# Kernel tuning notes

Hardware: AMD Instinct MI355X
Metric: run time of the kernel (lower is better)

Reference implementation:

```python
import jax, jax.numpy as jnp
import numpy as np

TOP_K = 2


def setup_inputs() -> dict:
    key = jax.random.key(0)
    ks = jax.random.split(key, 5)
    T, H, I, E = 4096, 2048, 4096, 8
    scale = 0.02
    return {
        "hidden_states": jax.random.normal(ks[0], (T, H), dtype=jnp.float32),
        "router_logits": jax.random.normal(ks[1], (T, E), dtype=jnp.float32),
        "w1": jax.random.normal(ks[2], (E, I, H), dtype=jnp.float32) * scale,
        "w3": jax.random.normal(ks[3], (E, I, H), dtype=jnp.float32) * scale,
        "w2": jax.random.normal(ks[4], (E, H, I), dtype=jnp.float32) * scale,
    }


def reference(hidden_states, router_logits, w1, w3, w2):
    # hidden_states: [T, H], router_logits: [T, E]
    E = w1.shape[0]
    # Top-k routing with softmax renormalization over the selected logits.
    topk_vals, topk_idx = jax.lax.top_k(router_logits, TOP_K)  # [T, K]
    routing_weights = jax.nn.softmax(topk_vals, axis=-1)       # [T, K]
    # combine[t, e] = sum of routing weights of slots that picked expert e
    combine = jnp.sum(
        jnp.where(topk_idx[:, :, None] == jnp.arange(E)[None, None, :],
                  routing_weights[:, :, None], 0.0),
        axis=1)  # [T, E]
    out = jnp.zeros_like(hidden_states)
    for e in range(E):  # fixed small structural loop over experts
        gate = hidden_states @ w1[e].T        # [T, I]
        up = hidden_states @ w3[e].T          # [T, I]
        y = (jax.nn.silu(gate) * up) @ w2[e].T  # [T, H]
        out = out + combine[:, e, None] * y
    return out
```

## Files before the change

### kernel.cpp

```cpp
#include <hip/hip_runtime.h>
#include <stdint.h>

#define T_TOK 4096
#define H_DIM 2048
#define I_DIM 4096
#define N_EXP 8

typedef __attribute__((ext_vector_type(8))) short bf16x8;
typedef __attribute__((ext_vector_type(4))) float f32x4;
typedef __attribute__((ext_vector_type(8))) unsigned short u16x8;

__device__ __forceinline__ unsigned short f2bf(float x) {
    union { float f; unsigned u; } v; v.f = x;
    unsigned r = v.u + 0x7FFF + ((v.u >> 16) & 1);
    return (unsigned short)(r >> 16);
}

__device__ __forceinline__ void async_cp16(const void* g, const unsigned short* lds_base) {
    __builtin_amdgcn_global_load_lds(
        (const __attribute__((address_space(1))) unsigned*)g,
        (__attribute__((address_space(3))) unsigned*)(unsigned)(uintptr_t)lds_base,
        16, 0, 0);
}

__global__ void routing_kernel(const float* __restrict__ logits,
                               int* __restrict__ counts, int* __restrict__ offsets,
                               int* __restrict__ btok, float* __restrict__ bw,
                               int* __restrict__ tok2slot) {
    __shared__ int s_cnt[N_EXP];
    __shared__ int s_off[N_EXP];
    __shared__ int s_cur[N_EXP];
    const int tid = threadIdx.x;
    if (tid < N_EXP) s_cnt[tid] = 0;
    __syncthreads();

    int e0a[16], e1a[16]; float w0a[16], w1a[16];
    #pragma unroll
    for (int it = 0; it < 16; ++it) {
        int t = tid + it * 256;
        float l[8];
        #pragma unroll
        for (int e = 0; e < 8; ++e) l[e] = logits[t * 8 + e];
        int b0 = 0; float v0 = l[0];
        #pragma unroll
        for (int e = 1; e < 8; ++e) if (l[e] > v0) { v0 = l[e]; b0 = e; }
        int b1 = (b0 == 0) ? 1 : 0; float v1 = l[b1];
        #pragma unroll
        for (int e = 0; e < 8; ++e) if (e != b0 && l[e] > v1) { v1 = l[e]; b1 = e; }
        float w0 = 1.0f / (1.0f + __expf(v1 - v0));
        e0a[it] = b0; e1a[it] = b1; w0a[it] = w0; w1a[it] = 1.0f - w0;
        atomicAdd(&s_cnt[b0], 1);
        atomicAdd(&s_cnt[b1], 1);
    }
    __syncthreads();
    if (tid == 0) {
        int acc = 0;
        for (int e = 0; e < N_EXP; ++e) { s_off[e] = acc; s_cur[e] = acc; acc += s_cnt[e]; }
    }
    __syncthreads();
    if (tid < N_EXP) { counts[tid] = s_cnt[tid]; offsets[tid] = s_off[tid]; }
    #pragma unroll
    for (int it = 0; it < 16; ++it) {
        int t = tid + it * 256;
        int p0 = atomicAdd(&s_cur[e0a[it]], 1);
        btok[p0] = t; bw[p0] = w0a[it];
        int p1 = atomicAdd(&s_cur[e1a[it]], 1);
        btok[p1] = t; bw[p1] = w1a[it];
        tok2slot[2 * t] = p0;
        tok2slot[2 * t + 1] = p1;
    }
}

__global__ void cvt_kernel(const float* __restrict__ x, unsigned short* __restrict__ xb) {
    int i = blockIdx.x * blockDim.x + threadIdx.x;
    float4 v = ((const float4*)x)[i];
    ushort4 o;
    o.x = f2bf(v.x); o.y = f2bf(v.y); o.z = f2bf(v.z); o.w = f2bf(v.w);
    ((ushort4*)xb)[i] = o;
}


__global__ __launch_bounds__(512, 2)
void gemm1p_kernel(const unsigned short* __restrict__ Xb,
                   const unsigned short* __restrict__ W1b,
                   const unsigned short* __restrict__ W3b,
                   const int* __restrict__ counts,
                   const int* __restrict__ offsets,
                   const int* __restrict__ btok,
                   unsigned short* __restrict__ hbuf) {
    const int e = blockIdx.z;
    const int ne = counts[e];
    const int mt = blockIdx.y;
    if (mt * 256 >= ne) return;
    const int nt = blockIdx.x;
    const int off = offsets[e];

    __shared__ unsigned short sA[3][256 * 32];
    __shared__ unsigned short sB1[3][128 * 32];
    __shared__ unsigned short sB3[3][128 * 32];
    __shared__ int s_tok[256];

    const int tid = threadIdx.x;
    if (tid < 256) {
        int slot = mt * 256 + tid;
        s_tok[tid] = btok[off + ((slot < ne) ? slot : (ne - 1))];
    }
    __syncthreads();

    const int lane = tid & 63;
    const int wv = tid >> 6;
    const int wm = (wv >> 1) << 6;
    const int wn = (wv & 1) << 6;
    const int q = lane >> 4;
    const int c = lane & 15;
    const int xq = q ^ ((c >> 1) & 3);

    const int aoff = (wm + c) * 32 + xq * 8;
    const int boff = (wn + c) * 32 + xq * 8;

    const int srow = wv * 16 + (lane >> 2);
    const int sg = (lane & 3) ^ ((lane >> 3) & 3);

    const unsigned short* gA0 = Xb + (size_t)s_tok[srow] * H_DIM + sg * 8;
    const unsigned short* gA1 = Xb + (size_t)s_tok[srow + 128] * H_DIM + sg * 8;
    const size_t wrow = (size_t)e * I_DIM + nt * 128 + srow;
    const unsigned short* gB1 = W1b + wrow * H_DIM + sg * 8;
    const unsigned short* gB3 = W3b + wrow * H_DIM + sg * 8;

    const int dofsA0 = wv * 512;
    const int dofsA1 = 4096 + wv * 512;
    const int dofsB  = wv * 512;

    f32x4 accg[4][4], accu[4][4];
    const f32x4 zero = {0.0f, 0.0f, 0.0f, 0.0f};
    #pragma unroll
    for (int i = 0; i < 4; ++i)
        #pragma unroll
        for (int j = 0; j < 4; ++j) { accg[i][j] = zero; accu[i][j] = zero; }

    async_cp16(gA0,      &sA[0][dofsA0]);
    async_cp16(gB1,      &sB1[0][dofsB]);
    async_cp16(gA1,      &sA[0][dofsA1]);
    async_cp16(gB3,      &sB3[0][dofsB]);
    async_cp16(gA0 + 32, &sA[1][dofsA0]);
    async_cp16(gB1 + 32, &sB1[1][dofsB]);
    async_cp16(gA1 + 32, &sA[1][dofsA1]);
    async_cp16(gB3 + 32, &sB3[1][dofsB]);
    asm volatile("s_waitcnt vmcnt(4)" ::: "memory");
    __builtin_amdgcn_s_barrier();
    __builtin_amdgcn_sched_barrier(0);

    const int NT = H_DIM / 32;
    for (int t = 0; t < NT; ++t) {
        const int cur = t % 3;
        const int nx2 = (t + 2) % 3;
        const bool stg = (t + 2) < NT;
        const int kt2 = (t + 2) * 32;

        bf16x8 af[4], b1f[4];
        #pragma unroll
        for (int i = 0; i < 4; ++i) af[i] = *(const bf16x8*)(&sA[cur][aoff + i * 512]);
        #pragma unroll
        for (int j = 0; j < 4; ++j) b1f[j] = *(const bf16x8*)(&sB1[cur][boff + j * 512]);
        if (stg) {
            async_cp16(gA0 + kt2, &sA[nx2][dofsA0]);
            async_cp16(gB1 + kt2, &sB1[nx2][dofsB]);
        }
        __builtin_amdgcn_s_barrier();
        __builtin_amdgcn_s_setprio(1);
        #pragma unroll
        for (int i = 0; i < 4; ++i)
            #pragma unroll
            for (int j = 0; j < 4; ++j)
                accg[i][j] = __builtin_amdgcn_mfma_f32_16x16x32_bf16(af[i], b1f[j], accg[i][j], 0, 0, 0);
        __builtin_amdgcn_s_setprio(0);
        __builtin_amdgcn_s_barrier();

        bf16x8 b3f[4];
        #pragma unroll
        for (int j = 0; j < 4; ++j) b3f[j] = *(const bf16x8*)(&sB3[cur][boff + j * 512]);
        if (stg) {
            async_cp16(gA1 + kt2, &sA[nx2][dofsA1]);
            async_cp16(gB3 + kt2, &sB3[nx2][dofsB]);
        }
        __builtin_amdgcn_s_barrier();
        __builtin_amdgcn_s_setprio(1);
        #pragma unroll
        for (int i = 0; i < 4; ++i)
            #pragma unroll
            for (int j = 0; j < 4; ++j)
                accu[i][j] = __builtin_amdgcn_mfma_f32_16x16x32_bf16(af[i], b3f[j], accu[i][j], 0, 0, 0);
        __builtin_amdgcn_s_setprio(0);

        if (t + 1 < NT) {
            if (stg) asm volatile("s_waitcnt vmcnt(4)" ::: "memory");
            else     asm volatile("s_waitcnt vmcnt(0)" ::: "memory");
            __builtin_amdgcn_s_barrier();
            __builtin_amdgcn_sched_barrier(0);
        }
    }

    #pragma unroll
    for (int i = 0; i < 4; ++i) {
        #pragma unroll
        for (int r = 0; r < 4; ++r) {
            int mloc = wm + i * 16 + q * 4 + r;
            int slot = mt * 256 + mloc;
            if (slot < ne) {
                size_t rowbase = (size_t)(off + slot) * I_DIM + nt * 128 + wn;
                #pragma unroll
                for (int j = 0; j < 4; ++j) {
                    float g = accg[i][j][r];
                    float u = accu[i][j][r];
                    float val = (g / (1.0f + __expf(-g))) * u;
                    hbuf[rowbase + j * 16 + c] = f2bf(val);
                }
            }
        }
    }
}

__global__ __launch_bounds__(512, 2)
void gemm2p_kernel(const unsigned short* __restrict__ hbuf,
                   const unsigned short* __restrict__ W2b,
                   const int* __restrict__ counts,
                   const int* __restrict__ offsets,
                   float* __restrict__ ybuf) {
    const int e = blockIdx.z;
    const int ne = counts[e];
    const int mt = blockIdx.y;
    if (mt * 256 >= ne) return;
    const int nt = blockIdx.x;
    const int off = offsets[e];

    __shared__ unsigned short sA[3][256 * 32];
    __shared__ unsigned short sB[3][256 * 32];

    const int tid = threadIdx.x;
    const int lane = tid & 63;
    const int wv = tid >> 6;
    const int wm = (wv >> 2) << 7;
    const int wn = (wv & 3) << 6;
    const int q = lane >> 4;
    const int c = lane & 15;
    const int xq = q ^ ((c >> 1) & 3);

    const int aoff = (wm + c) * 32 + xq * 8;
    const int boff = (wn + c) * 32 + xq * 8;

    const int srow = wv * 16 + (lane >> 2);
    const int sg = (lane & 3) ^ ((lane >> 3) & 3);

    int slot0 = mt * 256 + srow;        if (slot0 >= ne) slot0 = ne - 1;
    int slot1 = mt * 256 + srow + 128;  if (slot1 >= ne) slot1 = ne - 1;
    const unsigned short* gA0 = hbuf + (size_t)(off + slot0) * I_DIM + sg * 8;
    const unsigned short* gA1 = hbuf + (size_t)(off + slot1) * I_DIM + sg * 8;
    const size_t wrow = (size_t)e * H_DIM + nt * 256 + srow;
    const unsigned short* gB0 = W2b + wrow * I_DIM + sg * 8;
    const unsigned short* gB1 = W2b + (wrow + 128) * I_DIM + sg * 8;

    const int dofs0 = wv * 512;
    const int dofs1 = 4096 + wv * 512;

    f32x4 acc[8][4];
    const f32x4 zero = {0.0f, 0.0f, 0.0f, 0.0f};
    #pragma unroll
    for (int i = 0; i < 8; ++i)
        #pragma unroll
        for (int j = 0; j < 4; ++j) acc[i][j] = zero;

    async_cp16(gA0,      &sA[0][dofs0]);
    async_cp16(gB0,      &sB[0][dofs0]);
    async_cp16(gA1,      &sA[0][dofs1]);
    async_cp16(gB1,      &sB[0][dofs1]);
    async_cp16(gA0 + 32, &sA[1][dofs0]);
    async_cp16(gB0 + 32, &sB[1][dofs0]);
    async_cp16(gA1 + 32, &sA[1][dofs1]);
    async_cp16(gB1 + 32, &sB[1][dofs1]);
    asm volatile("s_waitcnt vmcnt(4)" ::: "memory");
    __builtin_amdgcn_s_barrier();
    __builtin_amdgcn_sched_barrier(0);

    const int NT = I_DIM / 32;
    for (int t = 0; t < NT; ++t) {
        const int cur = t % 3;
        const int nx2 = (t + 2) % 3;
        const bool stg = (t + 2) < NT;
        const int kt2 = (t + 2) * 32;

        bf16x8 af[4], bfr[4];
        #pragma unroll
        for (int i = 0; i < 4; ++i) af[i] = *(const bf16x8*)(&sA[cur][aoff + i * 512]);
        #pragma unroll
        for (int j = 0; j < 4; ++j) bfr[j] = *(const bf16x8*)(&sB[cur][boff + j * 512]);
        if (stg) {
            async_cp16(gA0 + kt2, &sA[nx2][dofs0]);
            async_cp16(gB0 + kt2, &sB[nx2][dofs0]);
        }
        __builtin_amdgcn_s_barrier();
        __builtin_amdgcn_s_setprio(1);
        #pragma unroll
        for (int i = 0; i < 4; ++i)
            #pragma unroll
            for (int j = 0; j < 4; ++j)
                acc[i][j] = __builtin_amdgcn_mfma_f32_16x16x32_bf16(af[i], bfr[j], acc[i][j], 0, 0, 0);
        __builtin_amdgcn_s_setprio(0);
        __builtin_amdgcn_s_barrier();

        bf16x8 af2[4];
        #pragma unroll
        for (int i = 0; i < 4; ++i) af2[i] = *(const bf16x8*)(&sA[cur][aoff + (i + 4) * 512]);
        if (stg) {
            async_cp16(gA1 + kt2, &sA[nx2][dofs1]);
            async_cp16(gB1 + kt2, &sB[nx2][dofs1]);
        }
        __builtin_amdgcn_s_barrier();
        __builtin_amdgcn_s_setprio(1);
        #pragma unroll
        for (int i = 0; i < 4; ++i)
            #pragma unroll
            for (int j = 0; j < 4; ++j)
                acc[i + 4][j] = __builtin_amdgcn_mfma_f32_16x16x32_bf16(af2[i], bfr[j], acc[i + 4][j], 0, 0, 0);
        __builtin_amdgcn_s_setprio(0);

        if (t + 1 < NT) {
            if (stg) asm volatile("s_waitcnt vmcnt(4)" ::: "memory");
            else     asm volatile("s_waitcnt vmcnt(0)" ::: "memory");
            __builtin_amdgcn_s_barrier();
            __builtin_amdgcn_sched_barrier(0);
        }
    }

    #pragma unroll
    for (int i = 0; i < 8; ++i) {
        #pragma unroll
        for (int r = 0; r < 4; ++r) {
            int mloc = wm + i * 16 + q * 4 + r;
            int slot = mt * 256 + mloc;
            if (slot < ne) {
                float* obase = ybuf + (size_t)(off + slot) * H_DIM + nt * 256 + wn;
                #pragma unroll
                for (int j = 0; j < 4; ++j)
                    obase[j * 16 + c] = acc[i][j][r];
            }
        }
    }
}

__global__ void combine_kernel(const float* __restrict__ ybuf,
                               const float* __restrict__ bw,
                               const int* __restrict__ tok2slot,
                               float* __restrict__ out) {
    int i = blockIdx.x * blockDim.x + threadIdx.x;
    int t = i >> 9;
    int h4 = i & 511;
    int p0 = tok2slot[2 * t], p1 = tok2slot[2 * t + 1];
    float w0 = bw[p0], w1 = bw[p1];
    float4 a = ((const float4*)(ybuf + (size_t)p0 * H_DIM))[h4];
    float4 b = ((const float4*)(ybuf + (size_t)p1 * H_DIM))[h4];
    float4 o;
    o.x = w0 * a.x + w1 * b.x;
    o.y = w0 * a.y + w1 * b.y;
    o.z = w0 * a.z + w1 * b.z;
    o.w = w0 * a.w + w1 * b.w;
    ((float4*)(out + (size_t)t * H_DIM))[h4] = o;
}


__global__ __launch_bounds__(256, 2)
void gemm1_kernel(const unsigned short* __restrict__ Xb,
                  const float* __restrict__ W1,
                  const float* __restrict__ W3,
                  const int* __restrict__ counts,
                  const int* __restrict__ offsets,
                  const int* __restrict__ btok,
                  unsigned short* __restrict__ hbuf) {
    const int e = blockIdx.z;
    const int ne = counts[e];
    const int mt = blockIdx.y;
    if (mt * 128 >= ne) return;
    const int nt = blockIdx.x;
    const int off = offsets[e];

    __shared__ unsigned short sA[128][32];
    __shared__ unsigned short sB1[128][32];
    __shared__ unsigned short sB3[128][32];
    __shared__ int s_tok[128];

    const int tid = threadIdx.x;
    if (tid < 128) {
        int slot = mt * 128 + tid;
        s_tok[tid] = (slot < ne) ? btok[off + slot] : -1;
    }

    const float* __restrict__ pB1 = W1 + (size_t)e * I_DIM * H_DIM + (size_t)(nt * 128) * H_DIM;
    const float* __restrict__ pB3 = W3 + (size_t)e * I_DIM * H_DIM + (size_t)(nt * 128) * H_DIM;

    const int lane = tid & 63;
    const int wv = tid >> 6;
    const int wm = (wv >> 1) << 6;
    const int wn = (wv & 1) << 6;
    const int q = lane >> 4;
    const int c = lane & 15;

    f32x4 accg[4][4], accu[4][4];
    const f32x4 zero = {0.0f, 0.0f, 0.0f, 0.0f};
    #pragma unroll
    for (int i = 0; i < 4; ++i)
        #pragma unroll
        for (int j = 0; j < 4; ++j) { accg[i][j] = zero; accu[i][j] = zero; }

    const int srow = tid >> 2;
    const int schunk = (tid & 3) * 8;

    for (int kt = 0; kt < H_DIM; kt += 32) {
        __syncthreads();
        #pragma unroll
        for (int p = 0; p < 2; ++p) {
            int r = srow + p * 64;
            int tok = s_tok[r];
            u16x8 av = {0, 0, 0, 0, 0, 0, 0, 0};
            if (tok >= 0)
                av = *(const u16x8*)(Xb + (size_t)tok * H_DIM + kt + schunk);
            *(u16x8*)(&sA[r][schunk]) = av;

            const float* b1 = pB1 + (size_t)r * H_DIM + kt + schunk;
            float4 x0 = *(const float4*)(b1);
            float4 x1 = *(const float4*)(b1 + 4);
            u16x8 bv;
            bv[0] = f2bf(x0.x); bv[1] = f2bf(x0.y); bv[2] = f2bf(x0.z); bv[3] = f2bf(x0.w);
            bv[4] = f2bf(x1.x); bv[5] = f2bf(x1.y); bv[6] = f2bf(x1.z); bv[7] = f2bf(x1.w);
            *(u16x8*)(&sB1[r][schunk]) = bv;

            const float* b3 = pB3 + (size_t)r * H_DIM + kt + schunk;
            float4 y0 = *(const float4*)(b3);
            float4 y1 = *(const float4*)(b3 + 4);
            u16x8 cv;
            cv[0] = f2bf(y0.x); cv[1] = f2bf(y0.y); cv[2] = f2bf(y0.z); cv[3] = f2bf(y0.w);
            cv[4] = f2bf(y1.x); cv[5] = f2bf(y1.y); cv[6] = f2bf(y1.z); cv[7] = f2bf(y1.w);
            *(u16x8*)(&sB3[r][schunk]) = cv;
        }
        __syncthreads();

        bf16x8 af[4], b1f[4], b3f[4];
        #pragma unroll
        for (int i = 0; i < 4; ++i)
            af[i] = *(const bf16x8*)(&sA[wm + i * 16 + c][q * 8]);
        #pragma unroll
        for (int j = 0; j < 4; ++j) {
            b1f[j] = *(const bf16x8*)(&sB1[wn + j * 16 + c][q * 8]);
            b3f[j] = *(const bf16x8*)(&sB3[wn + j * 16 + c][q * 8]);
        }
        #pragma unroll
        for (int i = 0; i < 4; ++i)
            #pragma unroll
            for (int j = 0; j < 4; ++j) {
                accg[i][j] = __builtin_amdgcn_mfma_f32_16x16x32_bf16(af[i], b1f[j], accg[i][j], 0, 0, 0);
                accu[i][j] = __builtin_amdgcn_mfma_f32_16x16x32_bf16(af[i], b3f[j], accu[i][j], 0, 0, 0);
            }
    }

    #pragma unroll
    for (int i = 0; i < 4; ++i) {
        #pragma unroll
        for (int r = 0; r < 4; ++r) {
            int mloc = wm + i * 16 + q * 4 + r;
            int slot = mt * 128 + mloc;
            if (slot < ne) {
                size_t rowbase = (size_t)(off + slot) * I_DIM + nt * 128 + wn;
                #pragma unroll
                for (int j = 0; j < 4; ++j) {
                    float g = accg[i][j][r];
                    float u = accu[i][j][r];
                    float val = (g / (1.0f + __expf(-g))) * u;
                    hbuf[rowbase + j * 16 + c] = f2bf(val);
                }
            }
        }
    }
}

__global__ __launch_bounds__(256, 2)
void gemm2_kernel(const unsigned short* __restrict__ hbuf,
                  const float* __restrict__ W2,
                  const int* __restrict__ counts,
                  const int* __restrict__ offsets,
                  const int* __restrict__ btok,
                  const float* __restrict__ bw,
                  float* __restrict__ out) {
    const int e = blockIdx.z;
    const int ne = counts[e];
    const int mt = blockIdx.y;
    if (mt * 128 >= ne) return;
    const int nt = blockIdx.x;
    const int off = offsets[e];

    __shared__ unsigned short sA[128][32];
    __shared__ unsigned short sB[128][32];

    const int tid = threadIdx.x;
    const int lane = tid & 63;
    const int wv = tid >> 6;
    const int wm = (wv >> 1) << 6;
    const int wn = (wv & 1) << 6;
    const int q = lane >> 4;
    const int c = lane & 15;

    const float* __restrict__ pB = W2 + (size_t)e * H_DIM * I_DIM + (size_t)(nt * 128) * I_DIM;

    f32x4 acc[4][4];
    const f32x4 zero = {0.0f, 0.0f, 0.0f, 0.0f};
    #pragma unroll
    for (int i = 0; i < 4; ++i)
        #pragma unroll
        for (int j = 0; j < 4; ++j) acc[i][j] = zero;

    const int srow = tid >> 2;
    const int schunk = (tid & 3) * 8;

    for (int kt = 0; kt < I_DIM; kt += 32) {
        __syncthreads();
        #pragma unroll
        for (int p = 0; p < 2; ++p) {
            int r = srow + p * 64;
            int slot = mt * 128 + r;
            u16x8 av = {0, 0, 0, 0, 0, 0, 0, 0};
            if (slot < ne)
                av = *(const u16x8*)(hbuf + (size_t)(off + slot) * I_DIM + kt + schunk);
            *(u16x8*)(&sA[r][schunk]) = av;

            const float* b = pB + (size_t)r * I_DIM + kt + schunk;
            float4 x0 = *(const float4*)(b);
            float4 x1 = *(const float4*)(b + 4);
            u16x8 bv;
            bv[0] = f2bf(x0.x); bv[1] = f2bf(x0.y); bv[2] = f2bf(x0.z); bv[3] = f2bf(x0.w);
            bv[4] = f2bf(x1.x); bv[5] = f2bf(x1.y); bv[6] = f2bf(x1.z); bv[7] = f2bf(x1.w);
            *(u16x8*)(&sB[r][schunk]) = bv;
        }
        __syncthreads();

        bf16x8 af[4], bfr[4];
        #pragma unroll
        for (int i = 0; i < 4; ++i)
            af[i] = *(const bf16x8*)(&sA[wm + i * 16 + c][q * 8]);
        #pragma unroll
        for (int j = 0; j < 4; ++j)
            bfr[j] = *(const bf16x8*)(&sB[wn + j * 16 + c][q * 8]);
        #pragma unroll
        for (int i = 0; i < 4; ++i)
            #pragma unroll
            for (int j = 0; j < 4; ++j)
                acc[i][j] = __builtin_amdgcn_mfma_f32_16x16x32_bf16(af[i], bfr[j], acc[i][j], 0, 0, 0);
    }

    #pragma unroll
    for (int i = 0; i < 4; ++i) {
        #pragma unroll
        for (int r = 0; r < 4; ++r) {
            int mloc = wm + i * 16 + q * 4 + r;
            int slot = mt * 128 + mloc;
            if (slot < ne) {
                int tok = btok[off + slot];
                float wgt = bw[off + slot];
                float* obase = out + (size_t)tok * H_DIM + nt * 128 + wn;
                #pragma unroll
                for (int j = 0; j < 4; ++j)
                    atomicAdd(obase + j * 16 + c, wgt * acc[i][j][r]);
            }
        }
    }
}


extern "C" void kernel_launch(void* const* d_in, const int* in_sizes, int n_in,
                              void* d_out, int out_size, void* d_ws, size_t ws_size,
                              hipStream_t stream) {
    const float* hs = (const float*)d_in[0];
    const float* rl = (const float*)d_in[1];
    const float* w1 = (const float*)d_in[2];
    const float* w3 = (const float*)d_in[3];
    const float* w2 = (const float*)d_in[4];
    float* out = (float*)d_out;

    char* ws = (char*)d_ws;
    int*   counts   = (int*)(ws);
    int*   offsets  = (int*)(ws + 256);
    int*   btok     = (int*)(ws + 4096);
    float* bw       = (float*)(ws + 36864);
    int*   tok2slot = (int*)(ws + 69632);

    const size_t MB = 1ull << 20;
    const size_t NEED_A = 529 * MB;

    if (ws_size >= NEED_A) {
        unsigned short* Xb   = (unsigned short*)(ws + 1 * MB);
        unsigned short* hbuf = (unsigned short*)(ws + 17 * MB);
        float*          ybuf = (float*)(ws + 81 * MB);
        unsigned short* w1b  = (unsigned short*)(ws + 145 * MB);
        unsigned short* w3b  = (unsigned short*)(ws + 273 * MB);
        unsigned short* w2b  = (unsigned short*)(ws + 401 * MB);

        routing_kernel<<<1, 256, 0, stream>>>(rl, counts, offsets, btok, bw, tok2slot);

        cvt_kernel<<<(T_TOK * H_DIM / 4) / 256, 256, 0, stream>>>(hs, Xb);
        int wn4 = N_EXP * I_DIM * H_DIM / 4;
        cvt_kernel<<<wn4 / 256, 256, 0, stream>>>(w1, w1b);
        cvt_kernel<<<wn4 / 256, 256, 0, stream>>>(w3, w3b);
        cvt_kernel<<<wn4 / 256, 256, 0, stream>>>(w2, w2b);

        gemm1p_kernel<<<dim3(I_DIM / 128, 32, N_EXP), 512, 0, stream>>>(
            Xb, w1b, w3b, counts, offsets, btok, hbuf);

        gemm2p_kernel<<<dim3(H_DIM / 256, 32, N_EXP), 512, 0, stream>>>(
            hbuf, w2b, counts, offsets, ybuf);

        combine_kernel<<<(T_TOK * (H_DIM / 4)) / 256, 256, 0, stream>>>(
            ybuf, bw, tok2slot, out);
    } else {
        unsigned short* Xb   = (unsigned short*)(ws + 1 * MB);
        unsigned short* hbuf = (unsigned short*)(ws + 32 * MB);

        hipMemsetAsync(out, 0, (size_t)T_TOK * H_DIM * sizeof(float), stream);

        routing_kernel<<<1, 256, 0, stream>>>(rl, counts, offsets, btok, bw, tok2slot);

        cvt_kernel<<<(T_TOK * H_DIM / 4) / 256, 256, 0, stream>>>(hs, Xb);

        gemm1_kernel<<<dim3(I_DIM / 128, T_TOK / 128, N_EXP), 256, 0, stream>>>(
            Xb, w1, w3, counts, offsets, btok, hbuf);

        gemm2_kernel<<<dim3(H_DIM / 128, T_TOK / 128, N_EXP), 256, 0, stream>>>(
            hbuf, w2, counts, offsets, btok, bw, out);
    }
}
```

Measured before the change: 1.276 ms.

## Deepen MoE GEMM pipelines to 4 stages and shrink gemm2 N-tile

Both grouped GEMM kernels move from a 3-buffer LDS ring with split half-iterations and extra barriers to a 4-buffer ring that prefetches three K-steps ahead, with one barrier per iteration. gemm1 reads token indices directly from global memory instead of staging them through shared memory with a syncthreads. gemm2's N tile drops from 256 to 128, so per-wave accumulators halve and the grid doubles. LDS use grows in gemm1, which may limit the two-blocks-per-CU occupancy, and the smaller gemm2 tile reloads the activation rows more often.

```diff
diff --git a/kernel.cpp b/kernel.cpp
--- a/kernel.cpp
+++ b/kernel.cpp
@@ -95,18 +95,11 @@
     const int nt = blockIdx.x;
     const int off = offsets[e];
 
-    __shared__ unsigned short sA[3][256 * 32];
-    __shared__ unsigned short sB1[3][128 * 32];
-    __shared__ unsigned short sB3[3][128 * 32];
-    __shared__ int s_tok[256];
+    __shared__ unsigned short sA[4][256 * 32];
+    __shared__ unsigned short sB1[4][128 * 32];
+    __shared__ unsigned short sB3[4][128 * 32];
 
     const int tid = threadIdx.x;
-    if (tid < 256) {
-        int slot = mt * 256 + tid;
-        s_tok[tid] = btok[off + ((slot < ne) ? slot : (ne - 1))];
-    }
-    __syncthreads();
-
     const int lane = tid & 63;
     const int wv = tid >> 6;
     const int wm = (wv >> 1) << 6;
@@ -121,8 +114,13 @@
     const int srow = wv * 16 + (lane >> 2);
     const int sg = (lane & 3) ^ ((lane >> 3) & 3);
 
-    const unsigned short* gA0 = Xb + (size_t)s_tok[srow] * H_DIM + sg * 8;
-    const unsigned short* gA1 = Xb + (size_t)s_tok[srow + 128] * H_DIM + sg * 8;
+    int sl0 = mt * 256 + srow;        if (sl0 >= ne) sl0 = ne - 1;
+    int sl1 = mt * 256 + srow + 128;  if (sl1 >= ne) sl1 = ne - 1;
+    const int tok0 = btok[off + sl0];
+    const int tok1 = btok[off + sl1];
+
+    const unsigned short* gA0 = Xb + (size_t)tok0 * H_DIM + sg * 8;
+    const unsigned short* gA1 = Xb + (size_t)tok1 * H_DIM + sg * 8;
     const size_t wrow = (size_t)e * I_DIM + nt * 128 + srow;
     const unsigned short* gB1 = W1b + wrow * H_DIM + sg * 8;
     const unsigned short* gB3 = W3b + wrow * H_DIM + sg * 8;
@@ -138,53 +136,48 @@
         #pragma unroll
         for (int j = 0; j < 4; ++j) { accg[i][j] = zero; accu[i][j] = zero; }
 
-    async_cp16(gA0,      &sA[0][dofsA0]);
-    async_cp16(gB1,      &sB1[0][dofsB]);
-    async_cp16(gA1,      &sA[0][dofsA1]);
-    async_cp16(gB3,      &sB3[0][dofsB]);
-    async_cp16(gA0 + 32, &sA[1][dofsA0]);
-    async_cp16(gB1 + 32, &sB1[1][dofsB]);
-    async_cp16(gA1 + 32, &sA[1][dofsA1]);
-    async_cp16(gB3 + 32, &sB3[1][dofsB]);
-    asm volatile("s_waitcnt vmcnt(4)" ::: "memory");
+    #pragma unroll
+    for (int h = 0; h < 3; ++h) {
+        const int k = h * 32;
+        async_cp16(gA0 + k, &sA[h][dofsA0]);
+        async_cp16(gA1 + k, &sA[h][dofsA1]);
+        async_cp16(gB1 + k, &sB1[h][dofsB]);
+        async_cp16(gB3 + k, &sB3[h][dofsB]);
+    }
+    asm volatile("s_waitcnt vmcnt(8)" ::: "memory");
     __builtin_amdgcn_s_barrier();
     __builtin_amdgcn_sched_barrier(0);
 
     const int NT = H_DIM / 32;
-    for (int t = 0; t < NT; ++t) {
-        const int cur = t % 3;
-        const int nx2 = (t + 2) % 3;
-        const bool stg = (t + 2) < NT;
-        const int kt2 = (t + 2) * 32;
-
-        bf16x8 af[4], b1f[4];
-        #pragma unroll
-        for (int i = 0; i < 4; ++i) af[i] = *(const bf16x8*)(&sA[cur][aoff + i * 512]);
-        #pragma unroll
-        for (int j = 0; j < 4; ++j) b1f[j] = *(const bf16x8*)(&sB1[cur][boff + j * 512]);
-        if (stg) {
-            async_cp16(gA0 + kt2, &sA[nx2][dofsA0]);
-            async_cp16(gB1 + kt2, &sB1[nx2][dofsB]);
-        }
-        __builtin_amdgcn_s_barrier();
+    #pragma unroll 4
+    for (int h = 0; h < NT; ++h) {
+        const unsigned short* pA  = sA[h & 3];
+        const unsigned short* pB1 = sB1[h & 3];
+        const unsigned short* pB3 = sB3[h & 3];
+
+        bf16x8 af[4], b1f[4], b3f[4];
+        #pragma unroll
+        for (int i = 0; i < 4; ++i) af[i]  = *(const bf16x8*)(pA  + aoff + i * 512);
+        #pragma unroll
+        for (int j = 0; j < 4; ++j) b1f[j] = *(const bf16x8*)(pB1 + boff + j * 512);
+        #pragma unroll
+        for (int j = 0; j < 4; ++j) b3f[j] = *(const bf16x8*)(pB3 + boff + j * 512);
+
+        if (h + 3 < NT) {
+            const int r3 = (h + 3) & 3;
+            const int k3 = (h + 3) * 32;
+            async_cp16(gA0 + k3, &sA[r3][dofsA0]);
+            async_cp16(gA1 + k3, &sA[r3][dofsA1]);
+            async_cp16(gB1 + k3, &sB1[r3][dofsB]);
+            async_cp16(gB3 + k3, &sB3[r3][dofsB]);
+        }
+
         __builtin_amdgcn_s_setprio(1);
         #pragma unroll
         for (int i = 0; i < 4; ++i)
             #pragma unroll
             for (int j = 0; j < 4; ++j)
                 accg[i][j] = __builtin_amdgcn_mfma_f32_16x16x32_bf16(af[i], b1f[j], accg[i][j], 0, 0, 0);
-        __builtin_amdgcn_s_setprio(0);
-        __builtin_amdgcn_s_barrier();
-
-        bf16x8 b3f[4];
-        #pragma unroll
-        for (int j = 0; j < 4; ++j) b3f[j] = *(const bf16x8*)(&sB3[cur][boff + j * 512]);
-        if (stg) {
-            async_cp16(gA1 + kt2, &sA[nx2][dofsA1]);
-            async_cp16(gB3 + kt2, &sB3[nx2][dofsB]);
-        }
-        __builtin_amdgcn_s_barrier();
-        __builtin_amdgcn_s_setprio(1);
         #pragma unroll
         for (int i = 0; i < 4; ++i)
             #pragma unroll
@@ -192,9 +185,10 @@
                 accu[i][j] = __builtin_amdgcn_mfma_f32_16x16x32_bf16(af[i], b3f[j], accu[i][j], 0, 0, 0);
         __builtin_amdgcn_s_setprio(0);
 
-        if (t + 1 < NT) {
-            if (stg) asm volatile("s_waitcnt vmcnt(4)" ::: "memory");
-            else     asm volatile("s_waitcnt vmcnt(0)" ::: "memory");
+        if (h + 1 < NT) {
+            if (h + 3 < NT)      asm volatile("s_waitcnt vmcnt(8)" ::: "memory");
+            else if (h + 2 < NT) asm volatile("s_waitcnt vmcnt(4)" ::: "memory");
+            else                 asm volatile("s_waitcnt vmcnt(0)" ::: "memory");
             __builtin_amdgcn_s_barrier();
             __builtin_amdgcn_sched_barrier(0);
         }
@@ -233,14 +227,14 @@
     const int nt = blockIdx.x;
     const int off = offsets[e];
 
-    __shared__ unsigned short sA[3][256 * 32];
-    __shared__ unsigned short sB[3][256 * 32];
+    __shared__ unsigned short sA[4][256 * 32];
+    __shared__ unsigned short sB[4][128 * 32];
 
     const int tid = threadIdx.x;
     const int lane = tid & 63;
     const int wv = tid >> 6;
-    const int wm = (wv >> 2) << 7;
-    const int wn = (wv & 3) << 6;
+    const int wm = (wv >> 1) << 6;
+    const int wn = (wv & 1) << 6;
     const int q = lane >> 4;
     const int c = lane & 15;
     const int xq = q ^ ((c >> 1) & 3);
@@ -255,49 +249,51 @@
     int slot1 = mt * 256 + srow + 128;  if (slot1 >= ne) slot1 = ne - 1;
     const unsigned short* gA0 = hbuf + (size_t)(off + slot0) * I_DIM + sg * 8;
     const unsigned short* gA1 = hbuf + (size_t)(off + slot1) * I_DIM + sg * 8;
-    const size_t wrow = (size_t)e * H_DIM + nt * 256 + srow;
-    const unsigned short* gB0 = W2b + wrow * I_DIM + sg * 8;
-    const unsigned short* gB1 = W2b + (wrow + 128) * I_DIM + sg * 8;
-
-    const int dofs0 = wv * 512;
-    const int dofs1 = 4096 + wv * 512;
-
-    f32x4 acc[8][4];
+    const size_t wrow = (size_t)e * H_DIM + nt * 128 + srow;
+    const unsigned short* gB = W2b + wrow * I_DIM + sg * 8;
+
+    const int dofsA0 = wv * 512;
+    const int dofsA1 = 4096 + wv * 512;
+    const int dofsB  = wv * 512;
+
+    f32x4 acc[4][4];
     const f32x4 zero = {0.0f, 0.0f, 0.0f, 0.0f};
     #pragma unroll
-    for (int i = 0; i < 8; ++i)
+    for (int i = 0; i < 4; ++i)
         #pragma unroll
         for (int j = 0; j < 4; ++j) acc[i][j] = zero;
 
-    async_cp16(gA0,      &sA[0][dofs0]);
-    async_cp16(gB0,      &sB[0][dofs0]);
-    async_cp16(gA1,      &sA[0][dofs1]);
-    async_cp16(gB1,      &sB[0][dofs1]);
-    async_cp16(gA0 + 32, &sA[1][dofs0]);
-    async_cp16(gB0 + 32, &sB[1][dofs0]);
-    async_cp16(gA1 + 32, &sA[1][dofs1]);
-    async_cp16(gB1 + 32, &sB[1][dofs1]);
-    asm volatile("s_waitcnt vmcnt(4)" ::: "memory");
+    #pragma unroll
+    for (int h = 0; h < 3; ++h) {
+        const int k = h * 32;
+        async_cp16(gA0 + k, &sA[h][dofsA0]);
+        async_cp16(gA1 + k, &sA[h][dofsA1]);
+        async_cp16(gB + k,  &sB[h][dofsB]);
+    }
+    asm volatile("s_waitcnt vmcnt(6)" ::: "memory");
     __builtin_amdgcn_s_barrier();
     __builtin_amdgcn_sched_barrier(0);
 
     const int NT = I_DIM / 32;
-    for (int t = 0; t < NT; ++t) {
-        const int cur = t % 3;
-        const int nx2 = (t + 2) % 3;
-        const bool stg = (t + 2) < NT;
-        const int kt2 = (t + 2) * 32;
+    #pragma unroll 4
+    for (int h = 0; h < NT; ++h) {
+        const unsigned short* pA = sA[h & 3];
+        const unsigned short* pB = sB[h & 3];
 
         bf16x8 af[4], bfr[4];
         #pragma unroll
-        for (int i = 0; i < 4; ++i) af[i] = *(const bf16x8*)(&sA[cur][aoff + i * 512]);
-        #pragma unroll
-        for (int j = 0; j < 4; ++j) bfr[j] = *(const bf16x8*)(&sB[cur][boff + j * 512]);
-        if (stg) {
-            async_cp16(gA0 + kt2, &sA[nx2][dofs0]);
-            async_cp16(gB0 + kt2, &sB[nx2][dofs0]);
-        }
-        __builtin_amdgcn_s_barrier();
+        for (int i = 0; i < 4; ++i) af[i]  = *(const bf16x8*)(pA + aoff + i * 512);
+        #pragma unroll
+        for (int j = 0; j < 4; ++j) bfr[j] = *(const bf16x8*)(pB + boff + j * 512);
+
+        if (h + 3 < NT) {
+            const int r3 = (h + 3) & 3;
+            const int k3 = (h + 3) * 32;
+            async_cp16(gA0 + k3, &sA[r3][dofsA0]);
+            async_cp16(gA1 + k3, &sA[r3][dofsA1]);
+            async_cp16(gB + k3,  &sB[r3][dofsB]);
+        }
+
         __builtin_amdgcn_s_setprio(1);
         #pragma unroll
         for (int i = 0; i < 4; ++i)
@@ -305,40 +301,24 @@
             for (int j = 0; j < 4; ++j)
                 acc[i][j] = __builtin_amdgcn_mfma_f32_16x16x32_bf16(af[i], bfr[j], acc[i][j], 0, 0, 0);
         __builtin_amdgcn_s_setprio(0);
-        __builtin_amdgcn_s_barrier();
-
-        bf16x8 af2[4];
-        #pragma unroll
-        for (int i = 0; i < 4; ++i) af2[i] = *(const bf16x8*)(&sA[cur][aoff + (i + 4) * 512]);
-        if (stg) {
-            async_cp16(gA1 + kt2, &sA[nx2][dofs1]);
-            async_cp16(gB1 + kt2, &sB[nx2][dofs1]);
-        }
-        __builtin_amdgcn_s_barrier();
-        __builtin_amdgcn_s_setprio(1);
-        #pragma unroll
-        for (int i = 0; i < 4; ++i)
-            #pragma unroll
-            for (int j = 0; j < 4; ++j)
-                acc[i + 4][j] = __builtin_amdgcn_mfma_f32_16x16x32_bf16(af2[i], bfr[j], acc[i + 4][j], 0, 0, 0);
-        __builtin_amdgcn_s_setprio(0);
-
-        if (t + 1 < NT) {
-            if (stg) asm volatile("s_waitcnt vmcnt(4)" ::: "memory");
-            else     asm volatile("s_waitcnt vmcnt(0)" ::: "memory");
+
+        if (h + 1 < NT) {
+            if (h + 3 < NT)      asm volatile("s_waitcnt vmcnt(6)" ::: "memory");
+            else if (h + 2 < NT) asm volatile("s_waitcnt vmcnt(3)" ::: "memory");
+            else                 asm volatile("s_waitcnt vmcnt(0)" ::: "memory");
             __builtin_amdgcn_s_barrier();
             __builtin_amdgcn_sched_barrier(0);
         }
     }
 
     #pragma unroll
-    for (int i = 0; i < 8; ++i) {
+    for (int i = 0; i < 4; ++i) {
         #pragma unroll
         for (int r = 0; r < 4; ++r) {
             int mloc = wm + i * 16 + q * 4 + r;
             int slot = mt * 256 + mloc;
             if (slot < ne) {
-                float* obase = ybuf + (size_t)(off + slot) * H_DIM + nt * 256 + wn;
+                float* obase = ybuf + (size_t)(off + slot) * H_DIM + nt * 128 + wn;
                 #pragma unroll
                 for (int j = 0; j < 4; ++j)
                     obase[j * 16 + c] = acc[i][j][r];
@@ -611,7 +591,7 @@
         gemm1p_kernel<<<dim3(I_DIM / 128, 32, N_EXP), 512, 0, stream>>>(
             Xb, w1b, w3b, counts, offsets, btok, hbuf);
 
-        gemm2p_kernel<<<dim3(H_DIM / 256, 32, N_EXP), 512, 0, stream>>>(
+        gemm2p_kernel<<<dim3(H_DIM / 128, 32, N_EXP), 512, 0, stream>>>(
             hbuf, w2b, counts, offsets, ybuf);
 
         combine_kernel<<<(T_TOK * (H_DIM / 4)) / 256, 256, 0, stream>>>(
```

Measured after the change: 1.249 ms. 2.1% less time.
